# Kernel optimization log

Hardware: AMD Instinct MI355X
Metric: run time of the kernel (lower is better)

## Reference

```python
import jax, jax.numpy as jnp
import numpy as np
from jax import lax

DIM = 384
HEADS = 8
PROMPTDIM = 192
EPS = 1e-12  # torch F.normalize eps


def conv1x1(x, w):
    # x: [b,c,h,w], w: [out,c]
    return jnp.einsum('bchw,oc->bohw', x, w)


def dwconv3x3(x, w):
    # depthwise 3x3, SAME padding; w: [C,1,3,3]
    return lax.conv_general_dilated(
        x, w, window_strides=(1, 1), padding='SAME',
        feature_group_count=x.shape[1],
        dimension_numbers=('NCHW', 'OIHW', 'NCHW'))


def setup_inputs() -> dict:
    key = jax.random.key(0)
    ks = jax.random.split(key, 8)
    b, h, w = 8, 128, 128
    s = 0.05
    return {
        'x': jax.random.normal(ks[0], (b, DIM, h, w), jnp.float32),
        'de': jax.random.normal(ks[1], (b, PROMPTDIM, h, w), jnp.float32),
        'w_qv': jax.random.normal(ks[2], (2 * DIM, DIM), jnp.float32) * s,
        'w_qv_dw': jax.random.normal(ks[3], (2 * DIM, 1, 3, 3), jnp.float32) * s,
        'w_k': jax.random.normal(ks[4], (DIM, PROMPTDIM), jnp.float32) * s,
        'w_k_dw': jax.random.normal(ks[5], (DIM, 1, 3, 3), jnp.float32) * s,
        'w_proj': jax.random.normal(ks[6], (DIM, DIM), jnp.float32) * s,
        'temperature': jnp.ones((HEADS, 1, 1), jnp.float32),
    }


def reference(x, de, w_qv, w_qv_dw, w_k, w_k_dw, w_proj, temperature):
    b, c, h, w = x.shape
    head_c = c // HEADS
    qv = dwconv3x3(conv1x1(x, w_qv), w_qv_dw)          # [b,2c,h,w]
    q, v = qv[:, :c], qv[:, c:]
    k = dwconv3x3(conv1x1(de, w_k), w_k_dw)            # [b,c,h,w]

    def to_heads(t):
        return t.reshape(b, HEADS, head_c, h * w)       # [b,head,c,hw]

    q, k, v = to_heads(q), to_heads(k), to_heads(v)
    # L2-normalize over hw (torch F.normalize: x / max(||x||, eps))
    q = q / jnp.maximum(jnp.linalg.norm(q, axis=-1, keepdims=True), EPS)
    k = k / jnp.maximum(jnp.linalg.norm(k, axis=-1, keepdims=True), EPS)
    attn = jnp.einsum('bhcs,bhds->bhcd', q, k) * temperature  # [b,head,c,c]
    attn = jax.nn.softmax(attn, axis=-1)
    out = jnp.einsum('bhcd,bhds->bhcs', attn, v)        # [b,head,c,hw]
    out = out.reshape(b, c, h, w)
    return conv1x1(out, w_proj)
```

## Files before the change

kernel.cpp:

```cpp
#include <hip/hip_runtime.h>

#define SPATIAL 16384
#define BATCH 8
#define CDIM 384
#define QVDIM 768
#define PDIM 192
#define NHEADS 8
#define HC 48

typedef __attribute__((ext_vector_type(8))) short short8;
typedef __attribute__((ext_vector_type(4))) float f32x4;
typedef __attribute__((ext_vector_type(4))) int i32x4;

__device__ __forceinline__ unsigned short f2bf(float f) {
  union { float f; unsigned u; } v; v.f = f;
  unsigned r = v.u + 0x7fffu + ((v.u >> 16) & 1u);
  return (unsigned short)(r >> 16);
}
__device__ __forceinline__ float bf2f(unsigned short h) {
  union { unsigned u; float f; } v; v.u = ((unsigned)h) << 16;
  return v.f;
}

__device__ __forceinline__ void gload16(const unsigned short* g, unsigned short* lds) {
  __builtin_amdgcn_global_load_lds(
      (const __attribute__((address_space(1))) void*)g,
      (__attribute__((address_space(3))) void*)lds,
      16, 0, 0);
}


__device__ __forceinline__ void w2bf_body(int bid, const float* __restrict__ in,
                                          unsigned short* __restrict__ out, int n) {
  int i = bid * 256 + threadIdx.x;
  if (i < n) out[i] = f2bf(in[i]);
}

__device__ __forceinline__ void transpose_body(int bid, const float* __restrict__ in,
                                               unsigned short* __restrict__ out, int C,
                                               float (*tile)[65]) {
  int st = bid % (SPATIAL / 64); bid /= (SPATIAL / 64);
  int ct = bid % (C / 64); int b = bid / (C / 64);
  int t = threadIdx.x;
  const float* ip = in + ((size_t)b * C + (size_t)ct * 64) * SPATIAL + (size_t)st * 64;
  int fx = t & 15, fy = t >> 4;
#pragma unroll
  for (int i = 0; i < 4; i++) {
    int r = fy + i * 16;
    f32x4 v = *(const f32x4*)(ip + (size_t)r * SPATIAL + fx * 4);
    tile[r][fx * 4 + 0] = v[0];
    tile[r][fx * 4 + 1] = v[1];
    tile[r][fx * 4 + 2] = v[2];
    tile[r][fx * 4 + 3] = v[3];
  }
  __syncthreads();
  unsigned short* op = out + ((size_t)b * SPATIAL + (size_t)st * 64) * C + (size_t)ct * 64;
  int cg = t & 7, sr = t >> 3;
#pragma unroll
  for (int i = 0; i < 2; i++) {
    int s = sr + i * 32;
    short8 o;
#pragma unroll
    for (int j = 0; j < 8; j++) o[j] = (short)f2bf(tile[cg * 8 + j][s]);
    *(short8*)(op + (size_t)s * C + cg * 8) = o;
  }
}

template<int BM, bool OUT_BF16>
__device__ __forceinline__ void gemm_body(int lbid, int nwg,
    const unsigned short* __restrict__ A, const unsigned short* __restrict__ B,
    void* __restrict__ Cv, int M, int K, long strideA, unsigned short* lds)
{
  constexpr int MFR = BM / 32;
  constexpr int ARD = BM / 64;
  constexpr int SL  = ARD + 4;
  constexpr int ASZ = BM * 64;
  constexpr int BUF = ASZ + 256 * 64;

  int bid = (lbid & 7) * (nwg >> 3) + (lbid >> 3);
  int mt = M / BM;
  int mb = bid % mt; bid /= mt;
  int nb = bid & 63; int b = bid >> 6;

  const unsigned short* Ab = A + (size_t)b * strideA + (size_t)mb * BM * K;
  const unsigned short* Bb = B + ((size_t)b * SPATIAL + (size_t)nb * 256) * K;

  int t = threadIdx.x;
  int lane = t & 63;
  int w = t >> 6;
  int wm = (w >> 2) * (BM / 2), wn = (w & 3) * 64;
  int lr = lane & 15, lg = lane >> 4;

  f32x4 acc[MFR][4];
#pragma unroll
  for (int i = 0; i < MFR; i++)
#pragma unroll
    for (int j = 0; j < 4; j++)
      acc[i][j] = (f32x4){0.f, 0.f, 0.f, 0.f};

  int arow = t >> 3;
  int aslot = (t & 7) ^ (arow & 7);
  const unsigned short* gA0 = Ab + (size_t)arow * K + aslot * 8;
  const unsigned short* gB0 = Bb + (size_t)arow * K + aslot * 8;

  auto STAGE = [&](int kt, int q) {
    int k0 = kt * 64;
    unsigned short* base = &lds[q * BUF];
#pragma unroll
    for (int r = 0; r < ARD; ++r)
      gload16(gA0 + (size_t)r * 64 * K + k0, base + r * 4096 + w * 512);
#pragma unroll
    for (int r = 0; r < 4; ++r)
      gload16(gB0 + (size_t)r * 64 * K + k0, base + ASZ + r * 4096 + w * 512);
  };

  int nt = K >> 6;
  STAGE(0, 0);
  STAGE(1, 1);

  int colr0 = ((0 * 4 + lg) ^ (lr & 7)) * 8;
  int colr1 = ((1 * 4 + lg) ^ (lr & 7)) * 8;

  for (int j = 0; j < nt; ++j) {
    if (j + 1 < nt) { asm volatile("s_waitcnt vmcnt(%0)" :: "n"(SL) : "memory"); }
    else            { asm volatile("s_waitcnt vmcnt(0)" ::: "memory"); }
    __builtin_amdgcn_s_barrier();
    __builtin_amdgcn_sched_barrier(0);

    unsigned short* cb = &lds[(j & 1) * BUF];

    {
      short8 af[MFR], bfv[4];
#pragma unroll
      for (int mi = 0; mi < MFR; ++mi)
        af[mi] = *(const short8*)(&cb[(wm + mi * 16 + lr) * 64 + colr0]);
#pragma unroll
      for (int ni = 0; ni < 4; ++ni)
        bfv[ni] = *(const short8*)(&cb[ASZ + (wn + ni * 16 + lr) * 64 + colr0]);
      __builtin_amdgcn_s_setprio(1);
#pragma unroll
      for (int mi = 0; mi < MFR; ++mi)
#pragma unroll
        for (int ni = 0; ni < 4; ++ni)
          acc[mi][ni] = __builtin_amdgcn_mfma_f32_16x16x32_bf16(af[mi], bfv[ni], acc[mi][ni], 0, 0, 0);
      __builtin_amdgcn_s_setprio(0);
    }
    __builtin_amdgcn_sched_barrier(0);
    {
      short8 af[MFR], bfv[4];
#pragma unroll
      for (int mi = 0; mi < MFR; ++mi)
        af[mi] = *(const short8*)(&cb[(wm + mi * 16 + lr) * 64 + colr1]);
#pragma unroll
      for (int ni = 0; ni < 4; ++ni)
        bfv[ni] = *(const short8*)(&cb[ASZ + (wn + ni * 16 + lr) * 64 + colr1]);
      __builtin_amdgcn_s_setprio(1);
#pragma unroll
      for (int mi = 0; mi < MFR; ++mi)
#pragma unroll
        for (int ni = 0; ni < 4; ++ni)
          acc[mi][ni] = __builtin_amdgcn_mfma_f32_16x16x32_bf16(af[mi], bfv[ni], acc[mi][ni], 0, 0, 0);
      __builtin_amdgcn_s_setprio(0);
    }
    __builtin_amdgcn_sched_barrier(0);
    __builtin_amdgcn_s_barrier();
    if (j + 2 < nt) STAGE(j + 2, j & 1);
  }

  size_t rbase = (size_t)mb * BM + wm + lg * 4;
  size_t cbase = (size_t)nb * 256 + wn + lr;
  if (OUT_BF16) {
    unsigned short* C = (unsigned short*)Cv + (size_t)b * M * SPATIAL;
#pragma unroll
    for (int mi = 0; mi < MFR; ++mi)
#pragma unroll
      for (int ni = 0; ni < 4; ++ni) {
        size_t r = rbase + mi * 16;
        size_t c = cbase + ni * 16;
#pragma unroll
        for (int jj = 0; jj < 4; ++jj)
          C[(r + jj) * SPATIAL + c] = f2bf(acc[mi][ni][jj]);
      }
  } else {
    float* C = (float*)Cv + (size_t)b * M * SPATIAL;
#pragma unroll
    for (int mi = 0; mi < MFR; ++mi)
#pragma unroll
      for (int ni = 0; ni < 4; ++ni) {
        size_t r = rbase + mi * 16;
        size_t c = cbase + ni * 16;
#pragma unroll
        for (int jj = 0; jj < 4; ++jj)
          C[(r + jj) * SPATIAL + c] = acc[mi][ni][jj];
      }
  }
}

template<bool NORM>
__device__ __forceinline__ void dwconv_body(int bid, const unsigned short* __restrict__ in,
    const float* __restrict__ wdw, unsigned short* __restrict__ out,
    float* __restrict__ norm2, int C, int in_cstride, int chan_off)
{
  int c = bid % C; int b = bid / C;
  const unsigned short* ip = in + ((size_t)b * in_cstride + chan_off + c) * SPATIAL;
  const float* wp = wdw + (size_t)(chan_off + c) * 9;
  float wr[9];
#pragma unroll
  for (int i = 0; i < 9; i++) wr[i] = wp[i];

  int t = threadIdx.x;
  int l = t & 63, g = t & 15;
  int y0 = (t >> 4) * 8;
  int xs = g * 8;
  unsigned short* op = out + ((size_t)b * C + c) * SPATIAL + y0 * 128 + xs;

  float rv[3][8], rl[3], rr[3];
  auto loadrow = [&](int yy, int s) {
    if ((unsigned)yy < 128u) {
      short8 cv = *(const short8*)(ip + yy * 128 + xs);
#pragma unroll
      for (int j = 0; j < 8; j++) rv[s][j] = bf2f((unsigned short)cv[j]);
    } else {
#pragma unroll
      for (int j = 0; j < 8; j++) rv[s][j] = 0.f;
    }
    float lf = __shfl(rv[s][7], (l - 1) & 63, 64);
    float rt = __shfl(rv[s][0], (l + 1) & 63, 64);
    rl[s] = (g == 0) ? 0.f : lf;
    rr[s] = (g == 15) ? 0.f : rt;
  };

  loadrow(y0 - 1, 0);
  loadrow(y0, 1);

  float sq = 0.f;
#pragma unroll
  for (int r = 0; r < 8; r++) {
    const int sp = r % 3, sc = (r + 1) % 3, sn = (r + 2) % 3;
    loadrow(y0 + r + 1, sn);
    float acc[8];
    acc[0] = wr[0]*rl[sp] + wr[1]*rv[sp][0] + wr[2]*rv[sp][1]
           + wr[3]*rl[sc] + wr[4]*rv[sc][0] + wr[5]*rv[sc][1]
           + wr[6]*rl[sn] + wr[7]*rv[sn][0] + wr[8]*rv[sn][1];
#pragma unroll
    for (int j = 1; j < 7; j++)
      acc[j] = wr[0]*rv[sp][j-1] + wr[1]*rv[sp][j] + wr[2]*rv[sp][j+1]
             + wr[3]*rv[sc][j-1] + wr[4]*rv[sc][j] + wr[5]*rv[sc][j+1]
             + wr[6]*rv[sn][j-1] + wr[7]*rv[sn][j] + wr[8]*rv[sn][j+1];
    acc[7] = wr[0]*rv[sp][6] + wr[1]*rv[sp][7] + wr[2]*rr[sp]
           + wr[3]*rv[sc][6] + wr[4]*rv[sc][7] + wr[5]*rr[sc]
           + wr[6]*rv[sn][6] + wr[7]*rv[sn][7] + wr[8]*rr[sn];
    short8 o;
#pragma unroll
    for (int j = 0; j < 8; j++) {
      o[j] = (short)f2bf(acc[j]);
      if (NORM) { float v = bf2f((unsigned short)o[j]); sq += v * v; }
    }
    *(short8*)(op + r * 128) = o;
  }

  if (NORM) {
#pragma unroll
    for (int off = 32; off > 0; off >>= 1) sq += __shfl_down(sq, off, 64);
    __shared__ float red[4];
    if (l == 0) red[t >> 6] = sq;
    __syncthreads();
    if (t == 0)
      norm2[(size_t)b * CDIM + c] = red[0] + red[1] + red[2] + red[3];
  }
}

__device__ __forceinline__ void dwt_body(int bid, const unsigned short* __restrict__ qv,
    const float* __restrict__ wdw, unsigned short* __restrict__ vT)
{
  __shared__ float tile[128][17];
  int yt = bid & 15; bid >>= 4;
  int ct = bid % 24; int b = bid / 24;
  int t = threadIdx.x;
  int l = t & 63, g = t & 15;
  int ci = t >> 4;
  int xs = g * 8;
  int y0 = yt * 8;
  int c = CDIM + ct * 16 + ci;
  const unsigned short* ip = qv + ((size_t)b * QVDIM + c) * SPATIAL;
  const float* wp = wdw + (size_t)c * 9;
  float wr[9];
#pragma unroll
  for (int i = 0; i < 9; i++) wr[i] = wp[i];

  float rv[3][8], rl[3], rr[3];
  auto loadrow = [&](int yy, int s) {
    if ((unsigned)yy < 128u) {
      short8 cv = *(const short8*)(ip + yy * 128 + xs);
#pragma unroll
      for (int j = 0; j < 8; j++) rv[s][j] = bf2f((unsigned short)cv[j]);
    } else {
#pragma unroll
      for (int j = 0; j < 8; j++) rv[s][j] = 0.f;
    }
    float lf = __shfl(rv[s][7], (l - 1) & 63, 64);
    float rt = __shfl(rv[s][0], (l + 1) & 63, 64);
    rl[s] = (g == 0) ? 0.f : lf;
    rr[s] = (g == 15) ? 0.f : rt;
  };

  loadrow(y0 - 1, 0);
  loadrow(y0, 1);

  int xw = t >> 1, cg = t & 1;
#pragma unroll
  for (int r = 0; r < 8; r++) {
    const int sp = r % 3, sc = (r + 1) % 3, sn = (r + 2) % 3;
    loadrow(y0 + r + 1, sn);
    float acc[8];
    acc[0] = wr[0]*rl[sp] + wr[1]*rv[sp][0] + wr[2]*rv[sp][1]
           + wr[3]*rl[sc] + wr[4]*rv[sc][0] + wr[5]*rv[sc][1]
           + wr[6]*rl[sn] + wr[7]*rv[sn][0] + wr[8]*rv[sn][1];
#pragma unroll
    for (int j = 1; j < 7; j++)
      acc[j] = wr[0]*rv[sp][j-1] + wr[1]*rv[sp][j] + wr[2]*rv[sp][j+1]
             + wr[3]*rv[sc][j-1] + wr[4]*rv[sc][j] + wr[5]*rv[sc][j+1]
             + wr[6]*rv[sn][j-1] + wr[7]*rv[sn][j] + wr[8]*rv[sn][j+1];
    acc[7] = wr[0]*rv[sp][6] + wr[1]*rv[sp][7] + wr[2]*rr[sp]
           + wr[3]*rv[sc][6] + wr[4]*rv[sc][7] + wr[5]*rr[sc]
           + wr[6]*rv[sn][6] + wr[7]*rv[sn][7] + wr[8]*rr[sn];
#pragma unroll
    for (int j = 0; j < 8; j++) tile[xs + j][ci] = acc[j];
    __syncthreads();
    short8 o;
#pragma unroll
    for (int j = 0; j < 8; j++) o[j] = (short)f2bf(tile[xw][cg * 8 + j]);
    *(short8*)(vT + ((size_t)b * SPATIAL + (size_t)(y0 + r) * 128 + xw) * CDIM + ct * 16 + cg * 8) = o;
    __syncthreads();
  }
}


#define PREP_N1 ((QVDIM * CDIM) / 256)
#define PREP_N2 ((CDIM * PDIM) / 256)
#define PREP_N3 (BATCH * (CDIM / 64) * (SPATIAL / 64))
#define PREP_N4 (BATCH * (PDIM / 64) * (SPATIAL / 64))
__global__ __launch_bounds__(256)
void k_prep(const float* __restrict__ w_qv, unsigned short* __restrict__ wqvb,
            const float* __restrict__ w_k, unsigned short* __restrict__ wkb,
            const float* __restrict__ x, unsigned short* __restrict__ xT,
            const float* __restrict__ de, unsigned short* __restrict__ deT)
{
  __shared__ float tile[64][65];
  int bid = blockIdx.x;
  if (bid < PREP_N1)                      w2bf_body(bid, w_qv, wqvb, QVDIM * CDIM);
  else if (bid < PREP_N1 + PREP_N2)       w2bf_body(bid - PREP_N1, w_k, wkb, CDIM * PDIM);
  else if (bid < PREP_N1 + PREP_N2 + PREP_N3)
    transpose_body(bid - PREP_N1 - PREP_N2, x, xT, CDIM, tile);
  else
    transpose_body(bid - PREP_N1 - PREP_N2 - PREP_N3, de, deT, PDIM, tile);
}

#define G1_N  (BATCH * (QVDIM / 256) * (SPATIAL / 256))
#define G1B_N (BATCH * (CDIM / 128) * (SPATIAL / 256))
__global__ __launch_bounds__(512, 2)
void k_gemms(const unsigned short* __restrict__ A1, const unsigned short* __restrict__ B1,
             void* __restrict__ C1,
             const unsigned short* __restrict__ A2, const unsigned short* __restrict__ B2,
             void* __restrict__ C2)
{
  __shared__ unsigned short lds[2 * (256 * 64 + 256 * 64)];
  int bid = blockIdx.x;
  if (bid < G1_N)
    gemm_body<256, true>(bid, G1_N, A1, B1, C1, QVDIM, CDIM, 0L, lds);
  else
    gemm_body<128, true>(bid - G1_N, G1B_N, A2, B2, C2, CDIM, PDIM, 0L, lds);
}

#define DW_NQ (BATCH * CDIM)
#define DW_NT (BATCH * 24 * 16)
#define DW_NK (BATCH * CDIM)
__global__ __launch_bounds__(256)
void k_dw(const unsigned short* __restrict__ qv, const unsigned short* __restrict__ kpre,
          const float* __restrict__ w_qvdw, const float* __restrict__ w_kdw,
          unsigned short* __restrict__ qdw, unsigned short* __restrict__ kdw,
          unsigned short* __restrict__ vT,
          float* __restrict__ n2q, float* __restrict__ n2k)
{
  int bid = blockIdx.x;
  if (bid < DW_NQ)
    dwconv_body<true>(bid, qv, w_qvdw, qdw, n2q, CDIM, QVDIM, 0);
  else if (bid < DW_NQ + DW_NT)
    dwt_body(bid - DW_NQ, qv, w_qvdw, vT);
  else
    dwconv_body<true>(bid - DW_NQ - DW_NT, kpre, w_kdw, kdw, n2k, CDIM, CDIM, 0);
}

__global__ __launch_bounds__(512, 2)
void k_gemm2(const unsigned short* __restrict__ A, const unsigned short* __restrict__ B,
             void* __restrict__ Cv)
{
  __shared__ unsigned short lds[2 * (128 * 64 + 256 * 64)];
  gemm_body<128, false>(blockIdx.x, gridDim.x, A, B, Cv, CDIM, CDIM, (long)(CDIM * CDIM), lds);
}

__global__ __launch_bounds__(256)
void k_logits(const unsigned short* __restrict__ qd, const unsigned short* __restrict__ kd,
              float* __restrict__ raw)
{
  int bid = blockIdx.x;
  int sp = bid & 15; bid >>= 4;
  int h = bid & 7; int b = bid >> 3;
  int lane = threadIdx.x & 63, wv = threadIdx.x >> 6;
  int lr = lane & 15, lg = lane >> 4;
  const unsigned short* qp = qd + ((size_t)b * CDIM + h * HC) * SPATIAL;
  const unsigned short* kp = kd + ((size_t)b * CDIM + h * HC) * SPATIAL;
  int s0 = sp * 1024 + wv * 256;
  f32x4 acc[3][3];
#pragma unroll
  for (int i = 0; i < 3; i++)
#pragma unroll
    for (int j = 0; j < 3; j++)
      acc[i][j] = (f32x4){0.f, 0.f, 0.f, 0.f};
  for (int ks = 0; ks < 256; ks += 32) {
    int off = s0 + ks + lg * 8;
    short8 qf[3], kf[3];
#pragma unroll
    for (int i = 0; i < 3; i++) {
      qf[i] = *(const short8*)(qp + (size_t)(i * 16 + lr) * SPATIAL + off);
      kf[i] = *(const short8*)(kp + (size_t)(i * 16 + lr) * SPATIAL + off);
    }
#pragma unroll
    for (int ci = 0; ci < 3; ci++)
#pragma unroll
      for (int di = 0; di < 3; di++)
        acc[ci][di] = __builtin_amdgcn_mfma_f32_16x16x32_bf16(qf[ci], kf[di], acc[ci][di], 0, 0, 0);
  }
  float* rp = raw + ((size_t)(b * NHEADS + h)) * HC * HC;
#pragma unroll
  for (int ci = 0; ci < 3; ci++)
#pragma unroll
    for (int di = 0; di < 3; di++)
#pragma unroll
      for (int j = 0; j < 4; j++)
        atomicAdd(&rp[(ci * 16 + lg * 4 + j) * HC + di * 16 + lr], acc[ci][di][j]);
}

__global__ void k_softmax(const float* __restrict__ raw, const float* __restrict__ n2q,
                          const float* __restrict__ n2k, const float* __restrict__ temp,
                          float* __restrict__ attn)
{
  int h = blockIdx.x & 7, b = blockIdx.x >> 3;
  int c = threadIdx.x;
  if (c >= HC) return;
  float tp = temp[h];
  float qn = fmaxf(sqrtf(n2q[b * CDIM + h * HC + c]), 1e-12f);
  const float* rp = raw + ((size_t)(b * NHEADS + h) * HC + c) * HC;
  float vals[HC];
  float mx = -1e30f;
#pragma unroll
  for (int d = 0; d < HC; d++) {
    float kn = fmaxf(sqrtf(n2k[b * CDIM + h * HC + d]), 1e-12f);
    float v = rp[d] * tp / (qn * kn);
    vals[d] = v;
    mx = fmaxf(mx, v);
  }
  float sum = 0.f;
#pragma unroll
  for (int d = 0; d < HC; d++) { vals[d] = expf(vals[d] - mx); sum += vals[d]; }
  float inv = 1.f / sum;
  float* ap = attn + ((size_t)(b * NHEADS + h) * HC + c) * HC;
#pragma unroll
  for (int d = 0; d < HC; d++) ap[d] = vals[d] * inv;
}

__global__ void k_mbuild(const float* __restrict__ attn, const float* __restrict__ wproj,
                         unsigned short* __restrict__ Mb)
{
  int o = blockIdx.x % CDIM, b = blockIdx.x / CDIM;
  int j = threadIdx.x;
  int h = j / HC, d = j % HC;
  const float* wp = wproj + (size_t)o * CDIM + h * HC;
  const float* ap = attn + (size_t)(b * NHEADS + h) * HC * HC + d;
  float s = 0.f;
#pragma unroll
  for (int cp = 0; cp < HC; cp++) s += wp[cp] * ap[cp * HC];
  Mb[((size_t)b * CDIM + o) * CDIM + j] = f2bf(s);
}

static const size_t OFF_QV   = 0;
static const size_t OFF_KDW  = 0;
static const size_t OFF_XT   = 201326592;
static const size_t OFF_QDW  = 201326592;
static const size_t OFF_DET  = 301989888;
static const size_t OFF_VT   = 301989888;
static const size_t OFF_KPRE = 402653184;
static const size_t OFF_WQVB = 503316480;
static const size_t OFF_WKB  = 503906304;
static const size_t OFF_N2Q  = 504053760;
static const size_t OFF_N2K  = 504066048;
static const size_t OFF_RAW  = 504078336;
static const size_t OFF_ATTN = 504668160;
static const size_t OFF_MB   = 505257984;

extern "C" void kernel_launch(void* const* d_in, const int* in_sizes, int n_in,
                              void* d_out, int out_size, void* d_ws, size_t ws_size,
                              hipStream_t stream) {
  const float* x      = (const float*)d_in[0];
  const float* de     = (const float*)d_in[1];
  const float* w_qv   = (const float*)d_in[2];
  const float* w_qvdw = (const float*)d_in[3];
  const float* w_k    = (const float*)d_in[4];
  const float* w_kdw  = (const float*)d_in[5];
  const float* w_proj = (const float*)d_in[6];
  const float* temp   = (const float*)d_in[7];

  char* ws = (char*)d_ws;
  unsigned short* qv    = (unsigned short*)(ws + OFF_QV);
  unsigned short* kdw   = (unsigned short*)(ws + OFF_KDW);
  unsigned short* xT    = (unsigned short*)(ws + OFF_XT);
  unsigned short* qdw   = (unsigned short*)(ws + OFF_QDW);
  unsigned short* deT   = (unsigned short*)(ws + OFF_DET);
  unsigned short* vT    = (unsigned short*)(ws + OFF_VT);
  unsigned short* kpre  = (unsigned short*)(ws + OFF_KPRE);
  unsigned short* wqvb  = (unsigned short*)(ws + OFF_WQVB);
  unsigned short* wkb   = (unsigned short*)(ws + OFF_WKB);
  float* n2q  = (float*)(ws + OFF_N2Q);
  float* n2k  = (float*)(ws + OFF_N2K);
  float* raw  = (float*)(ws + OFF_RAW);
  float* attn = (float*)(ws + OFF_ATTN);
  unsigned short* Mb = (unsigned short*)(ws + OFF_MB);

  hipMemsetAsync(ws + OFF_N2Q, 0, 12288 + 12288 + 589824, stream);

  k_prep<<<dim3(PREP_N1 + PREP_N2 + PREP_N3 + PREP_N4), dim3(256), 0, stream>>>(
      w_qv, wqvb, w_k, wkb, x, xT, de, deT);

  k_gemms<<<dim3(G1_N + G1B_N), dim3(512), 0, stream>>>(
      wqvb, xT, (void*)qv, wkb, deT, (void*)kpre);

  k_dw<<<dim3(DW_NQ + DW_NT + DW_NK), dim3(256), 0, stream>>>(
      qv, kpre, w_qvdw, w_kdw, qdw, kdw, vT, n2q, n2k);

  k_logits<<<dim3(BATCH * NHEADS * 16), dim3(256), 0, stream>>>(qdw, kdw, raw);
  k_softmax<<<dim3(BATCH * NHEADS), dim3(64), 0, stream>>>(raw, n2q, n2k, temp, attn);
  k_mbuild<<<dim3(BATCH * CDIM), dim3(CDIM), 0, stream>>>(attn, w_proj, Mb);

  k_gemm2<<<dim3(BATCH * (CDIM / 128) * (SPATIAL / 256)), dim3(512), 0, stream>>>(
      Mb, vT, d_out);
}
```

Measured before the change: 548.1 us.

## Shrink GEMM tiles to 128x128 with 256 threads and fuse softmax with M build

The GEMM body is generalised over BM, BN and thread count, and all three GEMMs switch from 256-wide spatial tiles on 512 threads to 128x128 tiles on 256 threads. This doubles the number of workgroups and halves LDS use per block. Separately, the softmax and Mb-build kernels are merged into one kernel per (batch, head) that keeps attn in LDS, removing the attn global round trip and one launch. The memset now zeroes only the logits buffer. The fused kernel runs only 64 blocks, each looping over 48 output chunks, so the projection-fold step has far less parallelism than the old 3072-block kernel.

```diff
diff --git a/kernel.cpp b/kernel.cpp
--- a/kernel.cpp
+++ b/kernel.cpp
@@ -66,29 +66,35 @@
   }
 }
 
-template<int BM, bool OUT_BF16>
+template<int BM, int BN, int NTHR, bool OUT_BF16>
 __device__ __forceinline__ void gemm_body(int lbid, int nwg,
     const unsigned short* __restrict__ A, const unsigned short* __restrict__ B,
     void* __restrict__ Cv, int M, int K, long strideA, unsigned short* lds)
 {
-  constexpr int MFR = BM / 32;
-  constexpr int ARD = BM / 64;
-  constexpr int SL  = ARD + 4;
-  constexpr int ASZ = BM * 64;
-  constexpr int BUF = ASZ + 256 * 64;
+  constexpr int NW   = NTHR / 64;
+  constexpr int NW_N = BN / 64;
+  constexpr int WM   = BM / (NW / NW_N);
+  constexpr int MFR  = WM / 16;
+  constexpr int RPR  = NTHR / 8;
+  constexpr int ARD  = BM / RPR;
+  constexpr int BRD  = BN / RPR;
+  constexpr int SL   = ARD + BRD;
+  constexpr int ASZ  = BM * 64;
+  constexpr int BUF  = ASZ + BN * 64;
+  constexpr int NB   = SPATIAL / BN;
 
   int bid = (lbid & 7) * (nwg >> 3) + (lbid >> 3);
   int mt = M / BM;
   int mb = bid % mt; bid /= mt;
-  int nb = bid & 63; int b = bid >> 6;
+  int nb = bid % NB; int b = bid / NB;
 
   const unsigned short* Ab = A + (size_t)b * strideA + (size_t)mb * BM * K;
-  const unsigned short* Bb = B + ((size_t)b * SPATIAL + (size_t)nb * 256) * K;
+  const unsigned short* Bb = B + ((size_t)b * SPATIAL + (size_t)nb * BN) * K;
 
   int t = threadIdx.x;
   int lane = t & 63;
   int w = t >> 6;
-  int wm = (w >> 2) * (BM / 2), wn = (w & 3) * 64;
+  int wm = (w / NW_N) * WM, wn = (w % NW_N) * 64;
   int lr = lane & 15, lg = lane >> 4;
 
   f32x4 acc[MFR][4];
@@ -108,10 +114,10 @@
     unsigned short* base = &lds[q * BUF];
 #pragma unroll
     for (int r = 0; r < ARD; ++r)
-      gload16(gA0 + (size_t)r * 64 * K + k0, base + r * 4096 + w * 512);
-#pragma unroll
-    for (int r = 0; r < 4; ++r)
-      gload16(gB0 + (size_t)r * 64 * K + k0, base + ASZ + r * 4096 + w * 512);
+      gload16(gA0 + (size_t)r * RPR * K + k0, base + r * (NTHR * 8) + w * 512);
+#pragma unroll
+    for (int r = 0; r < BRD; ++r)
+      gload16(gB0 + (size_t)r * RPR * K + k0, base + ASZ + r * (NTHR * 8) + w * 512);
   };
 
   int nt = K >> 6;
@@ -168,7 +174,7 @@
   }
 
   size_t rbase = (size_t)mb * BM + wm + lg * 4;
-  size_t cbase = (size_t)nb * 256 + wn + lr;
+  size_t cbase = (size_t)nb * BN + wn + lr;
   if (OUT_BF16) {
     unsigned short* C = (unsigned short*)Cv + (size_t)b * M * SPATIAL;
 #pragma unroll
@@ -356,20 +362,20 @@
     transpose_body(bid - PREP_N1 - PREP_N2 - PREP_N3, de, deT, PDIM, tile);
 }
 
-#define G1_N  (BATCH * (QVDIM / 256) * (SPATIAL / 256))
-#define G1B_N (BATCH * (CDIM / 128) * (SPATIAL / 256))
-__global__ __launch_bounds__(512, 2)
+#define G1_N  (BATCH * (QVDIM / 128) * (SPATIAL / 128))
+#define G1B_N (BATCH * (CDIM / 128) * (SPATIAL / 128))
+__global__ __launch_bounds__(256, 2)
 void k_gemms(const unsigned short* __restrict__ A1, const unsigned short* __restrict__ B1,
              void* __restrict__ C1,
              const unsigned short* __restrict__ A2, const unsigned short* __restrict__ B2,
              void* __restrict__ C2)
 {
-  __shared__ unsigned short lds[2 * (256 * 64 + 256 * 64)];
+  __shared__ unsigned short lds[2 * (128 * 64 + 128 * 64)];
   int bid = blockIdx.x;
   if (bid < G1_N)
-    gemm_body<256, true>(bid, G1_N, A1, B1, C1, QVDIM, CDIM, 0L, lds);
+    gemm_body<128, 128, 256, true>(bid, G1_N, A1, B1, C1, QVDIM, CDIM, 0L, lds);
   else
-    gemm_body<128, true>(bid - G1_N, G1B_N, A2, B2, C2, CDIM, PDIM, 0L, lds);
+    gemm_body<128, 128, 256, true>(bid - G1_N, G1B_N, A2, B2, C2, CDIM, PDIM, 0L, lds);
 }
 
 #define DW_NQ (BATCH * CDIM)
@@ -391,12 +397,13 @@
     dwconv_body<true>(bid - DW_NQ - DW_NT, kpre, w_kdw, kdw, n2k, CDIM, CDIM, 0);
 }
 
-__global__ __launch_bounds__(512, 2)
+__global__ __launch_bounds__(256, 2)
 void k_gemm2(const unsigned short* __restrict__ A, const unsigned short* __restrict__ B,
              void* __restrict__ Cv)
 {
-  __shared__ unsigned short lds[2 * (128 * 64 + 256 * 64)];
-  gemm_body<128, false>(blockIdx.x, gridDim.x, A, B, Cv, CDIM, CDIM, (long)(CDIM * CDIM), lds);
+  __shared__ unsigned short lds[2 * (128 * 64 + 128 * 64)];
+  gemm_body<128, 128, 256, false>(blockIdx.x, gridDim.x, A, B, Cv, CDIM, CDIM,
+                                  (long)(CDIM * CDIM), lds);
 }
 
 __global__ __launch_bounds__(256)
@@ -441,46 +448,50 @@
         atomicAdd(&rp[(ci * 16 + lg * 4 + j) * HC + di * 16 + lr], acc[ci][di][j]);
 }
 
-__global__ void k_softmax(const float* __restrict__ raw, const float* __restrict__ n2q,
-                          const float* __restrict__ n2k, const float* __restrict__ temp,
-                          float* __restrict__ attn)
-{
+__global__ __launch_bounds__(384)
+void k_smb(const float* __restrict__ raw, const float* __restrict__ n2q,
+           const float* __restrict__ n2k, const float* __restrict__ temp,
+           const float* __restrict__ wproj, unsigned short* __restrict__ Mb)
+{
+  __shared__ float attn_s[HC][HC];
+  __shared__ float kn_s[HC];
   int h = blockIdx.x & 7, b = blockIdx.x >> 3;
-  int c = threadIdx.x;
-  if (c >= HC) return;
-  float tp = temp[h];
-  float qn = fmaxf(sqrtf(n2q[b * CDIM + h * HC + c]), 1e-12f);
-  const float* rp = raw + ((size_t)(b * NHEADS + h) * HC + c) * HC;
-  float vals[HC];
-  float mx = -1e30f;
-#pragma unroll
-  for (int d = 0; d < HC; d++) {
-    float kn = fmaxf(sqrtf(n2k[b * CDIM + h * HC + d]), 1e-12f);
-    float v = rp[d] * tp / (qn * kn);
-    vals[d] = v;
-    mx = fmaxf(mx, v);
-  }
-  float sum = 0.f;
-#pragma unroll
-  for (int d = 0; d < HC; d++) { vals[d] = expf(vals[d] - mx); sum += vals[d]; }
-  float inv = 1.f / sum;
-  float* ap = attn + ((size_t)(b * NHEADS + h) * HC + c) * HC;
-#pragma unroll
-  for (int d = 0; d < HC; d++) ap[d] = vals[d] * inv;
-}
-
-__global__ void k_mbuild(const float* __restrict__ attn, const float* __restrict__ wproj,
-                         unsigned short* __restrict__ Mb)
-{
-  int o = blockIdx.x % CDIM, b = blockIdx.x / CDIM;
-  int j = threadIdx.x;
-  int h = j / HC, d = j % HC;
-  const float* wp = wproj + (size_t)o * CDIM + h * HC;
-  const float* ap = attn + (size_t)(b * NHEADS + h) * HC * HC + d;
-  float s = 0.f;
-#pragma unroll
-  for (int cp = 0; cp < HC; cp++) s += wp[cp] * ap[cp * HC];
-  Mb[((size_t)b * CDIM + o) * CDIM + j] = f2bf(s);
+  int t = threadIdx.x;
+
+  if (t < HC) kn_s[t] = fmaxf(sqrtf(n2k[b * CDIM + h * HC + t]), 1e-12f);
+  __syncthreads();
+
+  if (t < HC) {
+    int c = t;
+    float tp = temp[h];
+    float qn = fmaxf(sqrtf(n2q[b * CDIM + h * HC + c]), 1e-12f);
+    const float* rp = raw + ((size_t)(b * NHEADS + h) * HC + c) * HC;
+    float vals[HC];
+    float mx = -1e30f;
+#pragma unroll
+    for (int d = 0; d < HC; d++) {
+      float v = rp[d] * tp / (qn * kn_s[d]);
+      vals[d] = v;
+      mx = fmaxf(mx, v);
+    }
+    float sum = 0.f;
+#pragma unroll
+    for (int d = 0; d < HC; d++) { vals[d] = expf(vals[d] - mx); sum += vals[d]; }
+    float inv = 1.f / sum;
+#pragma unroll
+    for (int d = 0; d < HC; d++) attn_s[c][d] = vals[d] * inv;
+  }
+  __syncthreads();
+
+  for (int rep = 0; rep < 48; ++rep) {
+    int idx = rep * 384 + t;
+    int o = idx / HC, d = idx % HC;
+    const float* wp = wproj + (size_t)o * CDIM + h * HC;
+    float s = 0.f;
+#pragma unroll
+    for (int c = 0; c < HC; ++c) s += wp[c] * attn_s[c][d];
+    Mb[((size_t)b * CDIM + o) * CDIM + h * HC + d] = f2bf(s);
+  }
 }
 
 static const size_t OFF_QV   = 0;
@@ -495,7 +506,6 @@
 static const size_t OFF_N2Q  = 504053760;
 static const size_t OFF_N2K  = 504066048;
 static const size_t OFF_RAW  = 504078336;
-static const size_t OFF_ATTN = 504668160;
 static const size_t OFF_MB   = 505257984;
 
 extern "C" void kernel_launch(void* const* d_in, const int* in_sizes, int n_in,
@@ -523,24 +533,22 @@
   float* n2q  = (float*)(ws + OFF_N2Q);
   float* n2k  = (float*)(ws + OFF_N2K);
   float* raw  = (float*)(ws + OFF_RAW);
-  float* attn = (float*)(ws + OFF_ATTN);
   unsigned short* Mb = (unsigned short*)(ws + OFF_MB);
 
-  hipMemsetAsync(ws + OFF_N2Q, 0, 12288 + 12288 + 589824, stream);
+  hipMemsetAsync(ws + OFF_RAW, 0, 589824, stream);
 
   k_prep<<<dim3(PREP_N1 + PREP_N2 + PREP_N3 + PREP_N4), dim3(256), 0, stream>>>(
       w_qv, wqvb, w_k, wkb, x, xT, de, deT);
 
-  k_gemms<<<dim3(G1_N + G1B_N), dim3(512), 0, stream>>>(
+  k_gemms<<<dim3(G1_N + G1B_N), dim3(256), 0, stream>>>(
       wqvb, xT, (void*)qv, wkb, deT, (void*)kpre);
 
   k_dw<<<dim3(DW_NQ + DW_NT + DW_NK), dim3(256), 0, stream>>>(
       qv, kpre, w_qvdw, w_kdw, qdw, kdw, vT, n2q, n2k);
 
   k_logits<<<dim3(BATCH * NHEADS * 16), dim3(256), 0, stream>>>(qdw, kdw, raw);
-  k_softmax<<<dim3(BATCH * NHEADS), dim3(64), 0, stream>>>(raw, n2q, n2k, temp, attn);
-  k_mbuild<<<dim3(BATCH * CDIM), dim3(CDIM), 0, stream>>>(attn, w_proj, Mb);
-
-  k_gemm2<<<dim3(BATCH * (CDIM / 128) * (SPATIAL / 256)), dim3(512), 0, stream>>>(
+  k_smb<<<dim3(BATCH * NHEADS), dim3(384), 0, stream>>>(raw, n2q, n2k, temp, w_proj, Mb);
+
+  k_gemm2<<<dim3(BATCH * (CDIM / 128) * (SPATIAL / 128)), dim3(256), 0, stream>>>(
       Mb, vT, d_out);
 }
```

Result: slower. 602.0 us (+9.8%).
